# Optimization experiments

Measured on AMD Instinct MI355X. Metric: run time of the kernel, lower is better.

Reference implementation:

```python
import jax, jax.numpy as jnp
import numpy as np

N_NODES = 100000
N_EDGES = 3200000
N_IN = 5
N_OUT = 16


def setup_inputs() -> dict:
    key = jax.random.key(0)
    k1, k2, k3, k4 = jax.random.split(key, 4)
    atom = jax.random.normal(k1, (N_NODES, N_IN), dtype=jnp.float32)
    edge_index = jax.random.randint(k2, (2, N_EDGES), 0, N_NODES, dtype=jnp.int64)
    # Linear(n_input=5, n_neural=16) parameters
    W = jax.random.normal(k3, (N_OUT, N_IN), dtype=jnp.float32) / np.sqrt(N_IN)
    b = jax.random.normal(k4, (N_OUT,), dtype=jnp.float32) * 0.01
    return {"atom": atom, "edge_index": edge_index, "W": W, "b": b}


def reference(atom, edge_index, W, b):
    n = atom.shape[0]
    # add_self_loops
    loops = jnp.arange(n, dtype=edge_index.dtype)
    row = jnp.concatenate([edge_index[0], loops])  # source nodes [E+N]
    col = jnp.concatenate([edge_index[1], loops])  # target nodes [E+N]
    # x = Linear(atom)
    x = atom @ W.T + b  # [N, n_out]
    # degree over target index (includes self loops -> deg >= 1)
    deg = jax.ops.segment_sum(jnp.ones_like(col, dtype=x.dtype), col, num_segments=n)
    dis = deg ** -0.5  # deg_inv_sqrt, finite since deg >= 1
    norm = dis[row] * dis[col]  # [E+N]
    # gather-scale-scatter: message = norm * x_j, aggr='add' at col
    msgs = norm[:, None] * x[row]  # [E+N, n_out]
    out = jax.ops.segment_sum(msgs, col, num_segments=n)  # [N, n_out]
    return jax.nn.relu(out)
```

## Files before the change

### kernel.cpp

```cpp
#include <hip/hip_runtime.h>

#define N_IN 5
#define N_OUT 16
#define NB 256
#define BN 400
#define CAP 14336
#define BIN_MAGIC 10737419ull

__device__ __forceinline__ int bin_of(int c) {
    return (int)(((unsigned long long)(unsigned)c * BIN_MAGIC) >> 32);
}

__global__ __launch_bounds__(1024) void partition_kernel(
        const int* __restrict__ row, const int* __restrict__ col,
        int e, int* __restrict__ eb, int* __restrict__ cursor) {
    __shared__ int hist[NB];
    __shared__ int base[NB];
    int e4 = e >> 2;
    int nchunk = (e4 + 1023) / 1024;
    const int4* rowv = (const int4*)row;
    const int4* colv = (const int4*)col;
    for (int ch = blockIdx.x; ch < nchunk; ch += gridDim.x) {
        int i = ch * 1024 + threadIdx.x;
        bool valid = i < e4;
        int rr[4], cc[4], bb[4], pr[4];
        if (valid) {
            int4 r4 = rowv[i];
            int4 c4 = colv[i];
            rr[0] = r4.x; rr[1] = r4.y; rr[2] = r4.z; rr[3] = r4.w;
            cc[0] = c4.x; cc[1] = c4.y; cc[2] = c4.z; cc[3] = c4.w;
        }
        if (threadIdx.x < NB) hist[threadIdx.x] = 0;
        __syncthreads();
        if (valid) {
#pragma unroll
            for (int j = 0; j < 4; ++j) {
                bb[j] = bin_of(cc[j]);
                pr[j] = atomicAdd(&hist[bb[j]], 1);
            }
        }
        __syncthreads();
        if (threadIdx.x < NB) {
            int h = hist[threadIdx.x];
            base[threadIdx.x] = h ? atomicAdd(&cursor[threadIdx.x], h) : 0;
        }
        __syncthreads();
        if (valid) {
#pragma unroll
            for (int j = 0; j < 4; ++j) {
                int o = base[bb[j]] + pr[j];
                if (o < CAP)
                    eb[bb[j] * CAP + o] = ((cc[j] - bb[j] * BN) << 17) | rr[j];
            }
        }
        __syncthreads();
    }
    if (blockIdx.x == 0) {
        for (int i = (e4 << 2) + (int)threadIdx.x; i < e; i += (int)blockDim.x) {
            int c = col[i];
            int b = bin_of(c);
            int o = atomicAdd(&cursor[b], 1);
            if (o < CAP) eb[b * CAP + o] = ((c - b * BN) << 17) | row[i];
        }
    }
}

__global__ __launch_bounds__(1024) void deg_datom_kernel(
        const int* __restrict__ eb, const int* __restrict__ cursor,
        const float* __restrict__ atom,
        float4* __restrict__ datom8, int n) {
    __shared__ int hist[BN];
    int bin = blockIdx.x;
    if (threadIdx.x < BN) hist[threadIdx.x] = 0;
    __syncthreads();
    int s0 = bin * CAP;
    int cnt = min(max(cursor[bin], 0), CAP);
    const int4* ebv = (const int4*)(eb + s0);
    int cnt4 = cnt >> 2;
    for (int i = threadIdx.x; i < cnt4; i += 1024) {
        int4 v = ebv[i];
        atomicAdd(&hist[v.x >> 17], 1);
        atomicAdd(&hist[v.y >> 17], 1);
        atomicAdd(&hist[v.z >> 17], 1);
        atomicAdd(&hist[v.w >> 17], 1);
    }
    for (int i = (cnt4 << 2) + (int)threadIdx.x; i < cnt; i += 1024)
        atomicAdd(&hist[eb[s0 + i] >> 17], 1);
    __syncthreads();
    int l = threadIdx.x;
    if (l >= BN) return;
    int node = bin * BN + l;
    if (node >= n) return;
    float d = rsqrtf((float)(hist[l] + 1));
    const float* ap = atom + (size_t)node * N_IN;
    datom8[2 * node]     = make_float4(d * ap[0], d * ap[1], d * ap[2], d * ap[3]);
    datom8[2 * node + 1] = make_float4(d * ap[4], d, 0.0f, 0.0f);
}

__global__ __launch_bounds__(1024) void sort_gather_kernel(
        const int* __restrict__ eb, const int* __restrict__ cursor,
        const float4* __restrict__ datom8,
        const float* __restrict__ atom,
        const float* __restrict__ W, const float* __restrict__ bias,
        float* __restrict__ out, int n) {
    __shared__ int sebs[CAP];
    __shared__ int hist[BN];
    __shared__ int scanA[BN];
    __shared__ int scanB[BN];
    const int bin = blockIdx.x;
    const int tid = threadIdx.x;
    if (tid < BN) hist[tid] = 0;
    __syncthreads();
    const int s0 = bin * CAP;
    const int cnt = min(max(cursor[bin], 0), CAP);
    const int cnt4 = cnt >> 2;
    const int4* ebv = (const int4*)(eb + s0);

    int4 e0, e1, e2, e3, k0, k1, k2, k3;
    const bool v0 = tid          < cnt4;
    const bool v1 = tid + 1024   < cnt4;
    const bool v2 = tid + 2048   < cnt4;
    const bool v3 = tid + 3072   < cnt4;
    if (v0) { e0 = ebv[tid];
        k0.x = atomicAdd(&hist[e0.x >> 17], 1); k0.y = atomicAdd(&hist[e0.y >> 17], 1);
        k0.z = atomicAdd(&hist[e0.z >> 17], 1); k0.w = atomicAdd(&hist[e0.w >> 17], 1); }
    if (v1) { e1 = ebv[tid + 1024];
        k1.x = atomicAdd(&hist[e1.x >> 17], 1); k1.y = atomicAdd(&hist[e1.y >> 17], 1);
        k1.z = atomicAdd(&hist[e1.z >> 17], 1); k1.w = atomicAdd(&hist[e1.w >> 17], 1); }
    if (v2) { e2 = ebv[tid + 2048];
        k2.x = atomicAdd(&hist[e2.x >> 17], 1); k2.y = atomicAdd(&hist[e2.y >> 17], 1);
        k2.z = atomicAdd(&hist[e2.z >> 17], 1); k2.w = atomicAdd(&hist[e2.w >> 17], 1); }
    if (v3) { e3 = ebv[tid + 3072];
        k3.x = atomicAdd(&hist[e3.x >> 17], 1); k3.y = atomicAdd(&hist[e3.y >> 17], 1);
        k3.z = atomicAdd(&hist[e3.z >> 17], 1); k3.w = atomicAdd(&hist[e3.w >> 17], 1); }
    int tl = -1, tk = 0;
    if (tid < (cnt & 3)) {
        tl = eb[s0 + (cnt4 << 2) + tid];
        tk = atomicAdd(&hist[tl >> 17], 1);
    }
    __syncthreads();

    const int mydeg = (tid < BN) ? hist[tid] : 0;
    if (tid < BN) scanA[tid] = mydeg;
    __syncthreads();
    int* src = scanA; int* dst = scanB;
#pragma unroll
    for (int off = 1; off < 512; off <<= 1) {
        if (tid < BN) {
            int v = src[tid];
            if (tid >= off) v += src[tid - off];
            dst[tid] = v;
        }
        __syncthreads();
        int* t = src; src = dst; dst = t;
    }
    if (tid < BN) hist[tid] = src[tid] - mydeg;
    __syncthreads();

    if (v0) {
        sebs[hist[e0.x >> 17] + k0.x] = e0.x & 0x1FFFF;
        sebs[hist[e0.y >> 17] + k0.y] = e0.y & 0x1FFFF;
        sebs[hist[e0.z >> 17] + k0.z] = e0.z & 0x1FFFF;
        sebs[hist[e0.w >> 17] + k0.w] = e0.w & 0x1FFFF;
    }
    if (v1) {
        sebs[hist[e1.x >> 17] + k1.x] = e1.x & 0x1FFFF;
        sebs[hist[e1.y >> 17] + k1.y] = e1.y & 0x1FFFF;
        sebs[hist[e1.z >> 17] + k1.z] = e1.z & 0x1FFFF;
        sebs[hist[e1.w >> 17] + k1.w] = e1.w & 0x1FFFF;
    }
    if (v2) {
        sebs[hist[e2.x >> 17] + k2.x] = e2.x & 0x1FFFF;
        sebs[hist[e2.y >> 17] + k2.y] = e2.y & 0x1FFFF;
        sebs[hist[e2.z >> 17] + k2.z] = e2.z & 0x1FFFF;
        sebs[hist[e2.w >> 17] + k2.w] = e2.w & 0x1FFFF;
    }
    if (v3) {
        sebs[hist[e3.x >> 17] + k3.x] = e3.x & 0x1FFFF;
        sebs[hist[e3.y >> 17] + k3.y] = e3.y & 0x1FFFF;
        sebs[hist[e3.z >> 17] + k3.z] = e3.z & 0x1FFFF;
        sebs[hist[e3.w >> 17] + k3.w] = e3.w & 0x1FFFF;
    }
    if (tl >= 0) sebs[hist[tl >> 17] + tk] = tl & 0x1FFFF;
    __syncthreads();

    if (tid >= BN) return;
    const int node = bin * BN + tid;
    if (node >= n) return;
    const int st = hist[tid];
    float s0a = 0.f, s1a = 0.f, s2a = 0.f, s3a = 0.f, s4a = 0.f, s5a = 0.f;
#pragma unroll 4
    for (int i = 0; i < mydeg; ++i) {
        int r = sebs[st + i];
        float4 qa = datom8[2 * r];
        float4 qb = datom8[2 * r + 1];
        s0a += qa.x; s1a += qa.y; s2a += qa.z;
        s3a += qa.w; s4a += qb.x; s5a += qb.y;
    }
    const float d = rsqrtf((float)(mydeg + 1));
    const float* ap = atom + (size_t)node * N_IN;
    float t5[5];
    t5[0] = d * (s0a + d * ap[0]);
    t5[1] = d * (s1a + d * ap[1]);
    t5[2] = d * (s2a + d * ap[2]);
    t5[3] = d * (s3a + d * ap[3]);
    t5[4] = d * (s4a + d * ap[4]);
    const float t1 = d * (s5a + d);
    float ov[N_OUT];
#pragma unroll
    for (int o = 0; o < N_OUT; ++o) {
        float a = bias[o] * t1;
#pragma unroll
        for (int k = 0; k < 5; ++k) a = fmaf(W[o * N_IN + k], t5[k], a);
        ov[o] = fmaxf(a, 0.0f);
    }
    float4* op = (float4*)(out + (size_t)node * N_OUT);
#pragma unroll
    for (int q = 0; q < 4; ++q)
        op[q] = make_float4(ov[4 * q], ov[4 * q + 1], ov[4 * q + 2], ov[4 * q + 3]);
}

extern "C" void kernel_launch(void* const* d_in, const int* in_sizes, int n_in,
                              void* d_out, int out_size, void* d_ws, size_t ws_size,
                              hipStream_t stream) {
    const float* atom = (const float*)d_in[0];
    const int*   eidx = (const int*)d_in[1];
    const float* W    = (const float*)d_in[2];
    const float* b    = (const float*)d_in[3];
    float* out = (float*)d_out;

    int n = in_sizes[0] / N_IN;
    int e = in_sizes[1] / 2;
    const int* row = eidx;
    const int* col = eidx + e;

    auto align256 = [](size_t v) { return (v + 255) & ~(size_t)255; };
    char* w = (char*)d_ws;
    int*    cursor = (int*)w;     w += align256(NB * 4);
    int*    eb     = (int*)w;     w += align256((size_t)NB * CAP * 4);
    float4* datom8 = (float4*)w;

    hipMemsetAsync(cursor, 0, NB * sizeof(int), stream);
    partition_kernel<<<256, 1024, 0, stream>>>(row, col, e, eb, cursor);
    deg_datom_kernel<<<NB, 1024, 0, stream>>>(eb, cursor, atom, datom8, n);
    sort_gather_kernel<<<NB, 1024, 0, stream>>>(eb, cursor, datom8, atom, W, b, out, n);
}
```

Before: 132.0 us.

## Stage partition writes in LDS and split gather across all threads of block

The partition kernel now launches one block per chunk and sorts each chunk's edges by bin in shared memory before writing them out, so global writes per bin become contiguous runs. The gather phase in sort_gather now spreads the edges of a bin evenly over all 1024 threads instead of one thread per node. Each thread accumulates runs of the same target node and flushes them with shared-memory float atomics. This removes load imbalance from skewed degrees and idle threads above 400. It adds LDS atomics and lowers the per-bin edge cap to SCAP so the accumulator fits in shared memory, which could drop edges in bins that exceed it.

```diff
diff --git a/kernel.cpp b/kernel.cpp
--- a/kernel.cpp
+++ b/kernel.cpp
@@ -5,6 +5,7 @@
 #define NB 256
 #define BN 400
 #define CAP 14336
+#define SCAP 13584
 #define BIN_MAGIC 10737419ull
 
 __device__ __forceinline__ int bin_of(int c) {
@@ -14,53 +15,74 @@
 __global__ __launch_bounds__(1024) void partition_kernel(
         const int* __restrict__ row, const int* __restrict__ col,
         int e, int* __restrict__ eb, int* __restrict__ cursor) {
+    __shared__ int sEdge[4096];
+    __shared__ unsigned char sBinA[4096];
     __shared__ int hist[NB];
-    __shared__ int base[NB];
-    int e4 = e >> 2;
-    int nchunk = (e4 + 1023) / 1024;
-    const int4* rowv = (const int4*)row;
-    const int4* colv = (const int4*)col;
-    for (int ch = blockIdx.x; ch < nchunk; ch += gridDim.x) {
-        int i = ch * 1024 + threadIdx.x;
-        bool valid = i < e4;
-        int rr[4], cc[4], bb[4], pr[4];
-        if (valid) {
-            int4 r4 = rowv[i];
-            int4 c4 = colv[i];
-            rr[0] = r4.x; rr[1] = r4.y; rr[2] = r4.z; rr[3] = r4.w;
-            cc[0] = c4.x; cc[1] = c4.y; cc[2] = c4.z; cc[3] = c4.w;
-        }
-        if (threadIdx.x < NB) hist[threadIdx.x] = 0;
+    __shared__ int sA[NB];
+    __shared__ int sB[NB];
+    __shared__ int gbase[NB];
+    const int tid = threadIdx.x;
+    const int e4 = e >> 2;
+    const int i = blockIdx.x * 1024 + tid;
+    const bool valid = i < e4;
+    int rr[4], cc[4], bb[4], pr[4];
+    if (valid) {
+        int4 r4 = ((const int4*)row)[i];
+        int4 c4 = ((const int4*)col)[i];
+        rr[0] = r4.x; rr[1] = r4.y; rr[2] = r4.z; rr[3] = r4.w;
+        cc[0] = c4.x; cc[1] = c4.y; cc[2] = c4.z; cc[3] = c4.w;
+    }
+    if (tid < NB) hist[tid] = 0;
+    __syncthreads();
+    if (valid) {
+#pragma unroll
+        for (int j = 0; j < 4; ++j) {
+            bb[j] = bin_of(cc[j]);
+            pr[j] = atomicAdd(&hist[bb[j]], 1);
+        }
+    }
+    __syncthreads();
+    if (tid < NB) sA[tid] = hist[tid];
+    __syncthreads();
+    int* src = sA; int* dst = sB;
+#pragma unroll
+    for (int off = 1; off < NB; off <<= 1) {
+        if (tid < NB) {
+            int v = src[tid];
+            if (tid >= off) v += src[tid - off];
+            dst[tid] = v;
+        }
         __syncthreads();
-        if (valid) {
-#pragma unroll
-            for (int j = 0; j < 4; ++j) {
-                bb[j] = bin_of(cc[j]);
-                pr[j] = atomicAdd(&hist[bb[j]], 1);
-            }
-        }
-        __syncthreads();
-        if (threadIdx.x < NB) {
-            int h = hist[threadIdx.x];
-            base[threadIdx.x] = h ? atomicAdd(&cursor[threadIdx.x], h) : 0;
-        }
-        __syncthreads();
-        if (valid) {
-#pragma unroll
-            for (int j = 0; j < 4; ++j) {
-                int o = base[bb[j]] + pr[j];
-                if (o < CAP)
-                    eb[bb[j] * CAP + o] = ((cc[j] - bb[j] * BN) << 17) | rr[j];
-            }
-        }
-        __syncthreads();
+        int* t = src; src = dst; dst = t;
+    }
+    if (tid < NB) {
+        int h = hist[tid];
+        gbase[tid] = h ? atomicAdd(&cursor[tid], h) : 0;
+        dst[tid] = src[tid] - h;
+    }
+    __syncthreads();
+    int* startA = dst;
+    if (valid) {
+#pragma unroll
+        for (int j = 0; j < 4; ++j) {
+            int slot = startA[bb[j]] + pr[j];
+            sEdge[slot] = ((cc[j] - bb[j] * BN) << 17) | rr[j];
+            sBinA[slot] = (unsigned char)bb[j];
+        }
+    }
+    __syncthreads();
+    const int tot = src[NB - 1];
+    for (int s = tid; s < tot; s += 1024) {
+        int b = sBinA[s];
+        int pos = gbase[b] + (s - startA[b]);
+        if (pos < CAP) eb[b * CAP + pos] = sEdge[s];
     }
     if (blockIdx.x == 0) {
-        for (int i = (e4 << 2) + (int)threadIdx.x; i < e; i += (int)blockDim.x) {
-            int c = col[i];
+        for (int k = (e4 << 2) + tid; k < e; k += 1024) {
+            int c = col[k];
             int b = bin_of(c);
             int o = atomicAdd(&cursor[b], 1);
-            if (o < CAP) eb[b * CAP + o] = ((c - b * BN) << 17) | row[i];
+            if (o < CAP) eb[b * CAP + o] = ((c - b * BN) << 17) | row[k];
         }
     }
 }
@@ -103,16 +125,18 @@
         const float* __restrict__ atom,
         const float* __restrict__ W, const float* __restrict__ bias,
         float* __restrict__ out, int n) {
-    __shared__ int sebs[CAP];
-    __shared__ int hist[BN];
-    __shared__ int scanA[BN];
-    __shared__ int scanB[BN];
+    __shared__ int lds[16384];
+    int* sebs = lds;
+    int* hist = lds + SCAP;
+    int* sA   = lds + SCAP + 400;
+    int* sB   = lds + SCAP + 800;
+    float* sAcc = (float*)(lds + SCAP + 400);
     const int bin = blockIdx.x;
     const int tid = threadIdx.x;
     if (tid < BN) hist[tid] = 0;
     __syncthreads();
     const int s0 = bin * CAP;
-    const int cnt = min(max(cursor[bin], 0), CAP);
+    const int cnt = min(max(cursor[bin], 0), SCAP);
     const int cnt4 = cnt >> 2;
     const int4* ebv = (const int4*)(eb + s0);
 
@@ -141,9 +165,9 @@
     __syncthreads();
 
     const int mydeg = (tid < BN) ? hist[tid] : 0;
-    if (tid < BN) scanA[tid] = mydeg;
-    __syncthreads();
-    int* src = scanA; int* dst = scanB;
+    if (tid < BN) sA[tid] = mydeg;
+    __syncthreads();
+    int* src = sA; int* dst = sB;
 #pragma unroll
     for (int off = 1; off < 512; off <<= 1) {
         if (tid < BN) {
@@ -158,54 +182,81 @@
     __syncthreads();
 
     if (v0) {
-        sebs[hist[e0.x >> 17] + k0.x] = e0.x & 0x1FFFF;
-        sebs[hist[e0.y >> 17] + k0.y] = e0.y & 0x1FFFF;
-        sebs[hist[e0.z >> 17] + k0.z] = e0.z & 0x1FFFF;
-        sebs[hist[e0.w >> 17] + k0.w] = e0.w & 0x1FFFF;
+        sebs[hist[e0.x >> 17] + k0.x] = e0.x;
+        sebs[hist[e0.y >> 17] + k0.y] = e0.y;
+        sebs[hist[e0.z >> 17] + k0.z] = e0.z;
+        sebs[hist[e0.w >> 17] + k0.w] = e0.w;
     }
     if (v1) {
-        sebs[hist[e1.x >> 17] + k1.x] = e1.x & 0x1FFFF;
-        sebs[hist[e1.y >> 17] + k1.y] = e1.y & 0x1FFFF;
-        sebs[hist[e1.z >> 17] + k1.z] = e1.z & 0x1FFFF;
-        sebs[hist[e1.w >> 17] + k1.w] = e1.w & 0x1FFFF;
+        sebs[hist[e1.x >> 17] + k1.x] = e1.x;
+        sebs[hist[e1.y >> 17] + k1.y] = e1.y;
+        sebs[hist[e1.z >> 17] + k1.z] = e1.z;
+        sebs[hist[e1.w >> 17] + k1.w] = e1.w;
     }
     if (v2) {
-        sebs[hist[e2.x >> 17] + k2.x] = e2.x & 0x1FFFF;
-        sebs[hist[e2.y >> 17] + k2.y] = e2.y & 0x1FFFF;
-        sebs[hist[e2.z >> 17] + k2.z] = e2.z & 0x1FFFF;
-        sebs[hist[e2.w >> 17] + k2.w] = e2.w & 0x1FFFF;
+        sebs[hist[e2.x >> 17] + k2.x] = e2.x;
+        sebs[hist[e2.y >> 17] + k2.y] = e2.y;
+        sebs[hist[e2.z >> 17] + k2.z] = e2.z;
+        sebs[hist[e2.w >> 17] + k2.w] = e2.w;
     }
     if (v3) {
-        sebs[hist[e3.x >> 17] + k3.x] = e3.x & 0x1FFFF;
-        sebs[hist[e3.y >> 17] + k3.y] = e3.y & 0x1FFFF;
-        sebs[hist[e3.z >> 17] + k3.z] = e3.z & 0x1FFFF;
-        sebs[hist[e3.w >> 17] + k3.w] = e3.w & 0x1FFFF;
-    }
-    if (tl >= 0) sebs[hist[tl >> 17] + tk] = tl & 0x1FFFF;
+        sebs[hist[e3.x >> 17] + k3.x] = e3.x;
+        sebs[hist[e3.y >> 17] + k3.y] = e3.y;
+        sebs[hist[e3.z >> 17] + k3.z] = e3.z;
+        sebs[hist[e3.w >> 17] + k3.w] = e3.w;
+    }
+    if (tl >= 0) sebs[hist[tl >> 17] + tk] = tl;
+    for (int q = tid; q < 6 * BN; q += 1024) sAcc[q] = 0.0f;
+    __syncthreads();
+
+    const int ept = (cnt + 1023) >> 10;
+    int beg = tid * ept; if (beg > cnt) beg = cnt;
+    int end = beg + ept; if (end > cnt) end = cnt;
+    float a0 = 0.f, a1 = 0.f, a2 = 0.f, a3 = 0.f, a4 = 0.f, a5 = 0.f;
+    int cur = -1;
+    for (int ii = beg; ii < end; ++ii) {
+        int v = sebs[ii];
+        int l = v >> 17;
+        if (l != cur) {
+            if (cur >= 0) {
+                atomicAdd(&sAcc[cur * 6 + 0], a0);
+                atomicAdd(&sAcc[cur * 6 + 1], a1);
+                atomicAdd(&sAcc[cur * 6 + 2], a2);
+                atomicAdd(&sAcc[cur * 6 + 3], a3);
+                atomicAdd(&sAcc[cur * 6 + 4], a4);
+                atomicAdd(&sAcc[cur * 6 + 5], a5);
+            }
+            cur = l;
+            a0 = a1 = a2 = a3 = a4 = a5 = 0.f;
+        }
+        int r = v & 0x1FFFF;
+        float4 qa = datom8[2 * r];
+        float4 qb = datom8[2 * r + 1];
+        a0 += qa.x; a1 += qa.y; a2 += qa.z;
+        a3 += qa.w; a4 += qb.x; a5 += qb.y;
+    }
+    if (cur >= 0) {
+        atomicAdd(&sAcc[cur * 6 + 0], a0);
+        atomicAdd(&sAcc[cur * 6 + 1], a1);
+        atomicAdd(&sAcc[cur * 6 + 2], a2);
+        atomicAdd(&sAcc[cur * 6 + 3], a3);
+        atomicAdd(&sAcc[cur * 6 + 4], a4);
+        atomicAdd(&sAcc[cur * 6 + 5], a5);
+    }
     __syncthreads();
 
     if (tid >= BN) return;
     const int node = bin * BN + tid;
     if (node >= n) return;
-    const int st = hist[tid];
-    float s0a = 0.f, s1a = 0.f, s2a = 0.f, s3a = 0.f, s4a = 0.f, s5a = 0.f;
-#pragma unroll 4
-    for (int i = 0; i < mydeg; ++i) {
-        int r = sebs[st + i];
-        float4 qa = datom8[2 * r];
-        float4 qb = datom8[2 * r + 1];
-        s0a += qa.x; s1a += qa.y; s2a += qa.z;
-        s3a += qa.w; s4a += qb.x; s5a += qb.y;
-    }
     const float d = rsqrtf((float)(mydeg + 1));
     const float* ap = atom + (size_t)node * N_IN;
     float t5[5];
-    t5[0] = d * (s0a + d * ap[0]);
-    t5[1] = d * (s1a + d * ap[1]);
-    t5[2] = d * (s2a + d * ap[2]);
-    t5[3] = d * (s3a + d * ap[3]);
-    t5[4] = d * (s4a + d * ap[4]);
-    const float t1 = d * (s5a + d);
+    t5[0] = d * (sAcc[tid * 6 + 0] + d * ap[0]);
+    t5[1] = d * (sAcc[tid * 6 + 1] + d * ap[1]);
+    t5[2] = d * (sAcc[tid * 6 + 2] + d * ap[2]);
+    t5[3] = d * (sAcc[tid * 6 + 3] + d * ap[3]);
+    t5[4] = d * (sAcc[tid * 6 + 4] + d * ap[4]);
+    const float t1 = d * (sAcc[tid * 6 + 5] + d);
     float ov[N_OUT];
 #pragma unroll
     for (int o = 0; o < N_OUT; ++o) {
@@ -240,8 +291,11 @@
     int*    eb     = (int*)w;     w += align256((size_t)NB * CAP * 4);
     float4* datom8 = (float4*)w;
 
+    int nchunk = ((e >> 2) + 1023) / 1024;
+    if (nchunk < 1) nchunk = 1;
+
     hipMemsetAsync(cursor, 0, NB * sizeof(int), stream);
-    partition_kernel<<<256, 1024, 0, stream>>>(row, col, e, eb, cursor);
+    partition_kernel<<<nchunk, 1024, 0, stream>>>(row, col, e, eb, cursor);
     deg_datom_kernel<<<NB, 1024, 0, stream>>>(eb, cursor, atom, datom8, n);
     sort_gather_kernel<<<NB, 1024, 0, stream>>>(eb, cursor, datom8, atom, W, b, out, n);
 }
```

Result: no change. 132.3 us (+0.2%).
